# Optimization experiments

Measured on AMD Instinct MI355X. Metric: run time of the kernel, lower is better.

Reference implementation:

```python
import jax, jax.numpy as jnp
import numpy as np
import math

B, L, H, N, OUT, NPRED, NCTRL = 16, 4096, 512, 64, 256, 128, 64


def setup_inputs() -> dict:
    key = jax.random.key(0)
    ks = jax.random.split(key, 12)
    Nh = N // 2
    inp = jax.random.normal(ks[0], (B, L, H), dtype=jnp.float32)
    spec = jax.random.normal(ks[1], (B, L, NCTRL), dtype=jnp.float32)
    # S4DKernel params
    C = jax.random.normal(ks[2], (H, Nh, 2), dtype=jnp.float32)  # view_as_real of cfloat C
    log_dt = (jax.random.uniform(ks[3], (H,), dtype=jnp.float32)
              * (math.log(0.1) - math.log(0.001)) + math.log(0.001))
    log_A_real = jnp.log(0.5 * jnp.ones((H, Nh), dtype=jnp.float32))
    A_imag = math.pi * jnp.broadcast_to(jnp.arange(Nh, dtype=jnp.float32), (H, Nh))
    D = jax.random.normal(ks[4], (H,), dtype=jnp.float32)
    # output_linear: Conv1d(H, 2H, 1) then GLU(dim=-2)
    conv_w = jax.random.normal(ks[5], (2 * H, H), dtype=jnp.float32) / np.sqrt(H)
    conv_b = jax.random.normal(ks[6], (2 * H,), dtype=jnp.float32) * 0.01
    # output: Linear(in_len, out_len) applied on length axis
    out_w = jax.random.normal(ks[7], (OUT, L), dtype=jnp.float32) / np.sqrt(L)
    out_b = jax.random.normal(ks[8], (OUT,), dtype=jnp.float32) * 0.01
    return {"inp": inp, "spec": spec, "C": C, "log_dt": log_dt,
            "log_A_real": log_A_real, "A_imag": A_imag, "D": D,
            "conv_w": conv_w, "conv_b": conv_b, "out_w": out_w, "out_b": out_b}


def s4d_kernel(C, log_dt, log_A_real, A_imag, L):
    # Materialize SSM convolution kernel K: (H, L)
    dt = jnp.exp(log_dt)                                  # (H,)
    Cc = C[..., 0] + 1j * C[..., 1]                       # (H, N/2) complex
    A = -jnp.exp(log_A_real) + 1j * A_imag                # (H, N/2)
    dtA = A * dt[:, None]                                 # (H, N/2)
    # Vandermonde: exp(dtA * l) for l in [0, L)
    V = jnp.exp(dtA[:, :, None] * jnp.arange(L, dtype=jnp.float32))  # (H, N/2, L)
    Cc = Cc * (jnp.exp(dtA) - 1.0) / A                    # (H, N/2)
    K = 2.0 * jnp.einsum('hn,hnl->hl', Cc, V).real        # (H, L)
    return K


def reference(inp, spec, C, log_dt, log_A_real, A_imag, D, conv_w, conv_b, out_w, out_b):
    x = jnp.swapaxes(inp, -1, -2)                         # (B, H, L)
    Lx = x.shape[-1]
    k = s4d_kernel(C, log_dt, log_A_real, A_imag, Lx)     # (H, L)
    # FFT long convolution (linear conv via zero-padding to 2L)
    k_f = jnp.fft.rfft(k, n=2 * Lx)                       # (H, L+1)
    x_f = jnp.fft.rfft(x, n=2 * Lx)                       # (B, H, L+1)
    y = jnp.fft.irfft(x_f * k_f, n=2 * Lx)[..., :Lx]      # (B, H, L)
    y = y + x * D[:, None]                                # skip connection
    y = jax.nn.gelu(y, approximate=False)                 # torch nn.GELU default (erf)
    # Conv1d(k=1) + GLU over channel dim
    z = jnp.einsum('oh,bhl->bol', conv_w, y) + conv_b[:, None]  # (B, 2H, L)
    a, b = z[:, :H, :], z[:, H:, :]
    y = a * jax.nn.sigmoid(b)                             # (B, H, L)
    # Linear over length axis: L -> OUT
    y = jnp.einsum('bhl,ol->bho', y, out_w) + out_b       # (B, H, OUT)
    y = jnp.swapaxes(y, -1, -2)                           # (B, OUT, H)
    return y[:, :OUT, -NPRED:]
```

## Files before the change

### kernel.cpp

```cpp
#include <hip/hip_runtime.h>
#include <hip/hip_bf16.h>
#include <math.h>

#define B_     16
#define L_     4096
#define H_     512
#define NH     32
#define OUT_   256
#define NPRED_ 128
#define CCH    8
#define LCH    512

typedef __attribute__((ext_vector_type(8))) short bf16x8;
typedef __attribute__((ext_vector_type(4))) float f32x4;

__global__ void prep_kernel(const float* __restrict__ conv_w, const float* __restrict__ conv_b,
                            const float* __restrict__ out_w,
                            __hip_bfloat16* __restrict__ Wsel, float* __restrict__ bselp,
                            __hip_bfloat16* __restrict__ outw)
{
    int idx = blockIdx.x * blockDim.x + threadIdx.x;
    if (idx < 256 * 512) {
        int r = idx >> 9, hcol = idx & 511;
        int src = (r < 128) ? (384 + r) : (768 + r);
        Wsel[idx] = __float2bfloat16(conv_w[src * H_ + hcol]);
    } else if (idx < 256 * 512 + 256 * 4096) {
        int i2 = idx - 256 * 512;
        outw[i2] = __float2bfloat16(out_w[i2]);
    } else if (idx < 256 * 512 + 256 * 4096 + 256) {
        int r = idx - 256 * 512 - 256 * 4096;
        int src = (r < 128) ? (384 + r) : (768 + r);
        bselp[r] = conv_b[src];
    }
}

__global__ __launch_bounds__(256)
void scan_pass1(const float* __restrict__ inp, const float* __restrict__ log_dt,
                const float* __restrict__ log_A_real, const float* __restrict__ A_imag,
                float2* __restrict__ M)
{
    const int b = blockIdx.x, hg = blockIdx.y, c = blockIdx.z;
    const int h0 = hg * 32;
    const int tid = threadIdx.x;
    const int q = tid & 7, hl = tid >> 3, h = h0 + hl;

    __shared__ float xs[128][33];

    float wr[4], wi[4], sr[4] = {0,0,0,0}, si[4] = {0,0,0,0};
    const float dt = expf(log_dt[h]);
#pragma unroll
    for (int j = 0; j < 4; ++j) {
        const int n = q * 4 + j;
        const float Ar = -expf(log_A_real[h * NH + n]);
        const float Ai = A_imag[h * NH + n];
        const float er = expf(Ar * dt);
        wr[j] = er * cosf(Ai * dt);
        wi[j] = er * sinf(Ai * dt);
    }

    const size_t base = (size_t)b * L_ * H_ + (size_t)c * LCH * H_ + h0;
    for (int sub = 0; sub < 4; ++sub) {
#pragma unroll
        for (int k = 0; k < 16; ++k) {
            int idx = tid + k * 256;
            int ll = idx >> 5, hh = idx & 31;
            xs[ll][hh] = inp[base + (size_t)(sub * 128 + ll) * H_ + hh];
        }
        __syncthreads();
#pragma unroll 4
        for (int ll = 0; ll < 128; ++ll) {
            const float x = xs[ll][hl];
#pragma unroll
            for (int j = 0; j < 4; ++j) {
                const float nsr = fmaf(wr[j], sr[j], fmaf(-wi[j], si[j], x));
                const float nsi = fmaf(wr[j], si[j], wi[j] * sr[j]);
                sr[j] = nsr; si[j] = nsi;
            }
        }
        __syncthreads();
    }
#pragma unroll
    for (int j = 0; j < 4; ++j)
        M[(((size_t)b * CCH + c) * H_ + h) * NH + q * 4 + j] = make_float2(sr[j], si[j]);
}

__global__ __launch_bounds__(256)
void scan_pass2(const float* __restrict__ log_dt, const float* __restrict__ log_A_real,
                const float* __restrict__ A_imag, const float2* __restrict__ M,
                float2* __restrict__ Sin)
{
    const int idx = blockIdx.x * 256 + threadIdx.x;
    const int n = idx & 31, h = (idx >> 5) & 511, b = idx >> 14;
    const float dt = expf(log_dt[h]);
    const float Ar = -expf(log_A_real[h * NH + n]);
    const float Ai = A_imag[h * NH + n];
    const float er = expf(Ar * dt);
    float wr = er * cosf(Ai * dt), wi = er * sinf(Ai * dt);
#pragma unroll
    for (int s = 0; s < 9; ++s) {
        float nr = wr * wr - wi * wi;
        float ni = 2.0f * wr * wi;
        wr = nr; wi = ni;
    }
    float sre = 0.f, sim = 0.f;
#pragma unroll
    for (int c = 0; c < CCH; ++c) {
        const size_t mi_ = (((size_t)b * CCH + c) * H_ + h) * NH + n;
        float2 m = M[mi_];
        Sin[mi_] = make_float2(sre, sim);
        float nr = fmaf(wr, sre, fmaf(-wi, sim, m.x));
        float ni = fmaf(wr, sim, fmaf(wi, sre, m.y));
        sre = nr; sim = ni;
    }
}

__global__ __launch_bounds__(256)
void scan_pass3(const float* __restrict__ inp, const float* __restrict__ C,
                const float* __restrict__ log_dt, const float* __restrict__ log_A_real,
                const float* __restrict__ A_imag, const float* __restrict__ Dv,
                const float2* __restrict__ Sin, __hip_bfloat16* __restrict__ gT)
{
    const int b = blockIdx.x, hg = blockIdx.y, c = blockIdx.z;
    const int h0 = hg * 32;
    const int tid = threadIdx.x;
    const int q = tid & 7, hl = tid >> 3, h = h0 + hl;

    __shared__ float xs[128][33];
    __shared__ float ys[32][129];
    __shared__ float Ds[32];
    if (tid < 32) Ds[tid] = Dv[h0 + tid];

    const float dt = expf(log_dt[h]);
    float wr[4], wi[4], cr[4], cni[4], sr[4], si[4];
#pragma unroll
    for (int j = 0; j < 4; ++j) {
        const int n = q * 4 + j;
        const float Ar = -expf(log_A_real[h * NH + n]);
        const float Ai = A_imag[h * NH + n];
        const float er = expf(Ar * dt);
        const float wrr = er * cosf(Ai * dt);
        const float wii = er * sinf(Ai * dt);
        const float m2 = Ar * Ar + Ai * Ai;
        const float nr = wrr - 1.0f, nim = wii;
        const float qr = (nr * Ar + nim * Ai) / m2;
        const float qi = (nim * Ar - nr * Ai) / m2;
        const float Cr = C[(h * NH + n) * 2 + 0];
        const float Ci = C[(h * NH + n) * 2 + 1];
        wr[j]  = wrr;  wi[j] = wii;
        cr[j]  =  2.0f * (Cr * qr - Ci * qi);
        cni[j] = -2.0f * (Cr * qi + Ci * qr);
        float2 sv = Sin[(((size_t)b * CCH + c) * H_ + h) * NH + n];
        sr[j] = sv.x; si[j] = sv.y;
    }

    const size_t base = (size_t)b * L_ * H_ + (size_t)c * LCH * H_ + h0;
    __syncthreads();
    for (int sub = 0; sub < 4; ++sub) {
        const int l0 = c * LCH + sub * 128;
#pragma unroll
        for (int k = 0; k < 16; ++k) {
            int idx = tid + k * 256;
            int ll = idx >> 5, hh = idx & 31;
            xs[ll][hh] = inp[base + (size_t)(sub * 128 + ll) * H_ + hh];
        }
        __syncthreads();
#pragma unroll 4
        for (int ll = 0; ll < 128; ++ll) {
            const float x = xs[ll][hl];
            float y = 0.0f;
#pragma unroll
            for (int j = 0; j < 4; ++j) {
                const float nsr = fmaf(wr[j], sr[j], fmaf(-wi[j], si[j], x));
                const float nsi = fmaf(wr[j], si[j], wi[j] * sr[j]);
                sr[j] = nsr; si[j] = nsi;
                y = fmaf(cr[j], nsr, y);
                y = fmaf(cni[j], nsi, y);
            }
            y += __shfl_xor(y, 1);
            y += __shfl_xor(y, 2);
            y += __shfl_xor(y, 4);
            if (q == 0) ys[hl][ll] = y;
        }
        __syncthreads();
#pragma unroll
        for (int k = 0; k < 16; ++k) {
            int idx = tid + k * 256;
            int ll = idx >> 5, hh = idx & 31;
            float v = ys[hh][ll] + Ds[hh] * xs[ll][hh];
            float ge = 0.5f * v * (1.0f + erff(v * 0.70710678f));
            gT[((size_t)b * L_ + l0 + ll) * H_ + h0 + hh] = __float2bfloat16(ge);
        }
        __syncthreads();
    }
}

__device__ __forceinline__ unsigned short bf16bits(float f) {
    __hip_bfloat16 hv = __float2bfloat16(f);
    return *reinterpret_cast<unsigned short*>(&hv);
}

__global__ __launch_bounds__(512)
void gemm1_kernel(const __hip_bfloat16* __restrict__ gT, const __hip_bfloat16* __restrict__ Wsel,
                  const float* __restrict__ bsel, __hip_bfloat16* __restrict__ gated)
{
    const int b  = blockIdx.y;
    const int l0 = blockIdx.x * 128;
    const int tid = threadIdx.x;
    const int wid = tid >> 6, lane = tid & 63;
    const int wrr = wid >> 2;
    const int wcc = wid & 3;
    const int lr  = lane & 15;
    const int lk8 = (lane >> 4) * 8;

    __shared__ short As[128][40];
    __shared__ short Bs[256][40];

    f32x4 acc[4][4];
#pragma unroll
    for (int i = 0; i < 4; ++i)
#pragma unroll
        for (int j = 0; j < 4; ++j) acc[i][j] = (f32x4){0.f, 0.f, 0.f, 0.f};

    const short* gsrc = (const short*)gT + ((size_t)b * L_ + l0) * H_;
    const short* wsrc = (const short*)Wsel;
    const int arow = tid >> 2, aseg = tid & 3;

    for (int ks = 0; ks < 16; ++ks) {
        const int k0 = ks * 32;
        uint4 av  = *(const uint4*)(gsrc + (size_t)arow * H_ + k0 + aseg * 8);
        uint4 bv0 = *(const uint4*)(wsrc + (size_t)arow * 512 + k0 + aseg * 8);
        uint4 bv1 = *(const uint4*)(wsrc + (size_t)(arow + 128) * 512 + k0 + aseg * 8);
        *(uint4*)&As[arow][aseg * 8]       = av;
        *(uint4*)&Bs[arow][aseg * 8]       = bv0;
        *(uint4*)&Bs[arow + 128][aseg * 8] = bv1;
        __syncthreads();

        bf16x8 af[4], bfr[4];
#pragma unroll
        for (int mi = 0; mi < 4; ++mi)
            af[mi] = *(const bf16x8*)&As[wrr * 64 + mi * 16 + lr][lk8];
#pragma unroll
        for (int ni = 0; ni < 4; ++ni) {
            int col = (ni < 2) ? (wcc * 32 + ni * 16) : (128 + wcc * 32 + (ni - 2) * 16);
            bfr[ni] = *(const bf16x8*)&Bs[col + lr][lk8];
        }
#pragma unroll
        for (int mi = 0; mi < 4; ++mi)
#pragma unroll
            for (int ni = 0; ni < 4; ++ni)
                acc[mi][ni] = __builtin_amdgcn_mfma_f32_16x16x32_bf16(af[mi], bfr[ni], acc[mi][ni], 0, 0, 0);
        __syncthreads();
    }

    const int lj4 = (lane >> 4) * 4;
#pragma unroll
    for (int mi = 0; mi < 4; ++mi) {
#pragma unroll
        for (int ni = 0; ni < 2; ++ni) {
            const int oa = wcc * 32 + ni * 16 + lr;
            const float ba  = bsel[oa];
            const float bbv = bsel[oa + 128];
            ushort4 pack;
            unsigned short* pu = (unsigned short*)&pack;
#pragma unroll
            for (int j = 0; j < 4; ++j) {
                float za = acc[mi][ni][j] + ba;
                float zb = acc[mi][ni + 2][j] + bbv;
                float gv = za * (1.0f / (1.0f + expf(-zb)));
                pu[j] = bf16bits(gv);
            }
            const int lrow = l0 + wrr * 64 + mi * 16 + lj4;
            *(ushort4*)((unsigned short*)gated + ((size_t)b * NPRED_ + oa) * L_ + lrow) = pack;
        }
    }
}

__global__ __launch_bounds__(256)
void gemm2_kernel(const __hip_bfloat16* __restrict__ gated, const __hip_bfloat16* __restrict__ outw,
                  const float* __restrict__ outb, float* __restrict__ outp)
{
    const int b  = blockIdx.y;
    const int ot = blockIdx.x & 3, ht = blockIdx.x >> 2;
    const int o0 = ot * 64, hh0 = ht * 64;
    const int tid = threadIdx.x;
    const int wid = tid >> 6, lane = tid & 63;
    const int wrr = wid >> 1;
    const int wcc = wid & 1;
    const int lr  = lane & 15;
    const int lk8 = (lane >> 4) * 8;

    __shared__ short As[64][72];
    __shared__ short Bs[64][72];

    f32x4 acc[2][2];
#pragma unroll
    for (int i = 0; i < 2; ++i)
#pragma unroll
        for (int j = 0; j < 2; ++j) acc[i][j] = (f32x4){0.f, 0.f, 0.f, 0.f};

    const short* asrc = (const short*)gated + ((size_t)b * NPRED_ + hh0) * L_;
    const short* bsrc = (const short*)outw + (size_t)o0 * L_;
    const int row = tid >> 2, seg = tid & 3;

    for (int ks = 0; ks < 64; ++ks) {
        const int k0 = ks * 64;
        uint4 a0 = *(const uint4*)(asrc + (size_t)row * L_ + k0 + seg * 8);
        uint4 a1 = *(const uint4*)(asrc + (size_t)row * L_ + k0 + 32 + seg * 8);
        uint4 b0 = *(const uint4*)(bsrc + (size_t)row * L_ + k0 + seg * 8);
        uint4 b1 = *(const uint4*)(bsrc + (size_t)row * L_ + k0 + 32 + seg * 8);
        __syncthreads();
        *(uint4*)&As[row][seg * 8]      = a0;
        *(uint4*)&As[row][32 + seg * 8] = a1;
        *(uint4*)&Bs[row][seg * 8]      = b0;
        *(uint4*)&Bs[row][32 + seg * 8] = b1;
        __syncthreads();

#pragma unroll
        for (int kk = 0; kk < 2; ++kk) {
            bf16x8 af[2], bfv[2];
#pragma unroll
            for (int mi = 0; mi < 2; ++mi)
                af[mi] = *(const bf16x8*)&As[wrr * 32 + mi * 16 + lr][kk * 32 + lk8];
#pragma unroll
            for (int ni = 0; ni < 2; ++ni)
                bfv[ni] = *(const bf16x8*)&Bs[wcc * 32 + ni * 16 + lr][kk * 32 + lk8];
#pragma unroll
            for (int mi = 0; mi < 2; ++mi)
#pragma unroll
                for (int ni = 0; ni < 2; ++ni)
                    acc[mi][ni] = __builtin_amdgcn_mfma_f32_16x16x32_bf16(af[mi], bfv[ni], acc[mi][ni], 0, 0, 0);
        }
    }

    const int lj4 = (lane >> 4) * 4;
#pragma unroll
    for (int mi = 0; mi < 2; ++mi) {
#pragma unroll
        for (int ni = 0; ni < 2; ++ni) {
            const int og = o0 + wcc * 32 + ni * 16 + lr;
            const float bo = outb[og];
            float4 v;
            v.x = acc[mi][ni][0] + bo;
            v.y = acc[mi][ni][1] + bo;
            v.z = acc[mi][ni][2] + bo;
            v.w = acc[mi][ni][3] + bo;
            const int hh = hh0 + wrr * 32 + mi * 16 + lj4;
            *(float4*)(outp + ((size_t)b * OUT_ + og) * NPRED_ + hh) = v;
        }
    }
}

extern "C" void kernel_launch(void* const* d_in, const int* in_sizes, int n_in,
                              void* d_out, int out_size, void* d_ws, size_t ws_size,
                              hipStream_t stream)
{
    const float* inp        = (const float*)d_in[0];
    const float* C          = (const float*)d_in[2];
    const float* log_dt     = (const float*)d_in[3];
    const float* log_A_real = (const float*)d_in[4];
    const float* A_imag     = (const float*)d_in[5];
    const float* Dv         = (const float*)d_in[6];
    const float* conv_w     = (const float*)d_in[7];
    const float* conv_b     = (const float*)d_in[8];
    const float* out_w      = (const float*)d_in[9];
    const float* out_b      = (const float*)d_in[10];
    float* outp = (float*)d_out;

    const size_t off_Wsel  = 0;
    const size_t off_outw  = 262144;
    const size_t off_bsel  = 2359296;
    const size_t off_gT    = 2360320;
    const size_t off_gated = 69469184;
    const size_t off_M     = off_gT;
    const size_t off_Sin   = off_gated;
    const size_t need      = 86246400;
    if (ws_size < need) return;

    char* ws = (char*)d_ws;
    __hip_bfloat16* Wsel  = (__hip_bfloat16*)(ws + off_Wsel);
    __hip_bfloat16* outw  = (__hip_bfloat16*)(ws + off_outw);
    float*          bselp = (float*)(ws + off_bsel);
    __hip_bfloat16* gT    = (__hip_bfloat16*)(ws + off_gT);
    __hip_bfloat16* gated = (__hip_bfloat16*)(ws + off_gated);
    float2*         M     = (float2*)(ws + off_M);
    float2*         Sin   = (float2*)(ws + off_Sin);

    const int prep_total = 256 * 512 + 256 * 4096 + 256;
    prep_kernel<<<(prep_total + 255) / 256, 256, 0, stream>>>(conv_w, conv_b, out_w, Wsel, bselp, outw);
    scan_pass1<<<dim3(16, 16, CCH), 256, 0, stream>>>(inp, log_dt, log_A_real, A_imag, M);
    scan_pass2<<<1024, 256, 0, stream>>>(log_dt, log_A_real, A_imag, M, Sin);
    scan_pass3<<<dim3(16, 16, CCH), 256, 0, stream>>>(inp, C, log_dt, log_A_real, A_imag, Dv, Sin, gT);
    gemm1_kernel<<<dim3(32, 16), 512, 0, stream>>>(gT, Wsel, bselp, gated);
    gemm2_kernel<<<dim3(8, 16), 256, 0, stream>>>(gated, outw, out_b, outp);
}
```

Before: 612.6 us.

## Remap scan threads to 16 modes per lane and drop shared-memory staging

Reworks the chunked SSM scan kernels so each wavefront owns one length chunk, with each lane holding 16 complex modes for one channel instead of 4. Inputs are read directly from global memory through a small register prefetch queue, which removes the shared-memory tiles and block barriers. In pass 3 the output reduction becomes a single cross-half shuffle, and GELU is written straight to gT per row. Pass 2 now updates M in place, so the separate Sin buffer is gone. The cost is higher register pressure (about 96 live floats per thread), 32-wide strided global loads per row, and fewer blocks in the launch grid.

Result: slower. 808.2 us (+31.9%).

```diff
diff --git a/kernel.cpp b/kernel.cpp
--- a/kernel.cpp
+++ b/kernel.cpp
@@ -39,55 +39,56 @@
                 const float* __restrict__ log_A_real, const float* __restrict__ A_imag,
                 float2* __restrict__ M)
 {
-    const int b = blockIdx.x, hg = blockIdx.y, c = blockIdx.z;
-    const int h0 = hg * 32;
+    const int b = blockIdx.x, hg = blockIdx.y, cq = blockIdx.z;
     const int tid = threadIdx.x;
-    const int q = tid & 7, hl = tid >> 3, h = h0 + hl;
-
-    __shared__ float xs[128][33];
-
-    float wr[4], wi[4], sr[4] = {0,0,0,0}, si[4] = {0,0,0,0};
+    const int wv = tid >> 6, lane = tid & 63;
+    const int c = cq * 4 + wv;
+    const int hl = lane & 31, nh0 = (lane >> 5) * 16;
+    const int h = hg * 32 + hl;
+
+    float wr[16], wi[16], sr[16], si[16];
     const float dt = expf(log_dt[h]);
 #pragma unroll
-    for (int j = 0; j < 4; ++j) {
-        const int n = q * 4 + j;
+    for (int j = 0; j < 16; ++j) {
+        const int n = nh0 + j;
         const float Ar = -expf(log_A_real[h * NH + n]);
         const float Ai = A_imag[h * NH + n];
         const float er = expf(Ar * dt);
         wr[j] = er * cosf(Ai * dt);
         wi[j] = er * sinf(Ai * dt);
-    }
-
-    const size_t base = (size_t)b * L_ * H_ + (size_t)c * LCH * H_ + h0;
-    for (int sub = 0; sub < 4; ++sub) {
-#pragma unroll
-        for (int k = 0; k < 16; ++k) {
-            int idx = tid + k * 256;
-            int ll = idx >> 5, hh = idx & 31;
-            xs[ll][hh] = inp[base + (size_t)(sub * 128 + ll) * H_ + hh];
-        }
-        __syncthreads();
+        sr[j] = 0.f; si[j] = 0.f;
+    }
+
+    const float* xp = inp + ((size_t)b * L_ + (size_t)c * LCH) * H_ + h;
+    float xq0 = xp[0 * (size_t)H_];
+    float xq1 = xp[1 * (size_t)H_];
+    float xq2 = xp[2 * (size_t)H_];
+    float xq3 = xp[3 * (size_t)H_];
 #pragma unroll 4
-        for (int ll = 0; ll < 128; ++ll) {
-            const float x = xs[ll][hl];
-#pragma unroll
-            for (int j = 0; j < 4; ++j) {
-                const float nsr = fmaf(wr[j], sr[j], fmaf(-wi[j], si[j], x));
-                const float nsi = fmaf(wr[j], si[j], wi[j] * sr[j]);
-                sr[j] = nsr; si[j] = nsi;
-            }
-        }
-        __syncthreads();
-    }
-#pragma unroll
-    for (int j = 0; j < 4; ++j)
-        M[(((size_t)b * CCH + c) * H_ + h) * NH + q * 4 + j] = make_float2(sr[j], si[j]);
+    for (int l = 0; l < LCH; ++l) {
+        int lp = l + 4; lp = (lp < LCH) ? lp : (LCH - 1);
+        const float xf = xp[(size_t)lp * H_];
+        const float x = xq0;
+#pragma unroll
+        for (int j = 0; j < 16; ++j) {
+            const float nsr = fmaf(wr[j], sr[j], fmaf(-wi[j], si[j], x));
+            const float nsi = fmaf(wr[j], si[j], wi[j] * sr[j]);
+            sr[j] = nsr; si[j] = nsi;
+        }
+        xq0 = xq1; xq1 = xq2; xq2 = xq3; xq3 = xf;
+    }
+
+    float2* Mp = M + (((size_t)b * CCH + c) * H_ + h) * NH + nh0;
+#pragma unroll
+    for (int j = 0; j < 16; j += 2) {
+        float4 v; v.x = sr[j]; v.y = si[j]; v.z = sr[j + 1]; v.w = si[j + 1];
+        *(float4*)&Mp[j] = v;
+    }
 }
 
 __global__ __launch_bounds__(256)
 void scan_pass2(const float* __restrict__ log_dt, const float* __restrict__ log_A_real,
-                const float* __restrict__ A_imag, const float2* __restrict__ M,
-                float2* __restrict__ Sin)
+                const float* __restrict__ A_imag, float2* __restrict__ M)
 {
     const int idx = blockIdx.x * 256 + threadIdx.x;
     const int n = idx & 31, h = (idx >> 5) & 511, b = idx >> 14;
@@ -107,7 +108,7 @@
     for (int c = 0; c < CCH; ++c) {
         const size_t mi_ = (((size_t)b * CCH + c) * H_ + h) * NH + n;
         float2 m = M[mi_];
-        Sin[mi_] = make_float2(sre, sim);
+        M[mi_] = make_float2(sre, sim);
         float nr = fmaf(wr, sre, fmaf(-wi, sim, m.x));
         float ni = fmaf(wr, sim, fmaf(wi, sre, m.y));
         sre = nr; sim = ni;
@@ -120,21 +121,19 @@
                 const float* __restrict__ A_imag, const float* __restrict__ Dv,
                 const float2* __restrict__ Sin, __hip_bfloat16* __restrict__ gT)
 {
-    const int b = blockIdx.x, hg = blockIdx.y, c = blockIdx.z;
-    const int h0 = hg * 32;
+    const int b = blockIdx.x, hg = blockIdx.y, cq = blockIdx.z;
     const int tid = threadIdx.x;
-    const int q = tid & 7, hl = tid >> 3, h = h0 + hl;
-
-    __shared__ float xs[128][33];
-    __shared__ float ys[32][129];
-    __shared__ float Ds[32];
-    if (tid < 32) Ds[tid] = Dv[h0 + tid];
-
+    const int wv = tid >> 6, lane = tid & 63;
+    const int c = cq * 4 + wv;
+    const int hl = lane & 31, nh0 = (lane >> 5) * 16;
+    const int h = hg * 32 + hl;
+
+    float wr[16], wi[16], cr[16], cni[16], sr[16], si[16];
     const float dt = expf(log_dt[h]);
-    float wr[4], wi[4], cr[4], cni[4], sr[4], si[4];
-#pragma unroll
-    for (int j = 0; j < 4; ++j) {
-        const int n = q * 4 + j;
+    const float2* Sp = Sin + (((size_t)b * CCH + c) * H_ + h) * NH + nh0;
+#pragma unroll
+    for (int j = 0; j < 16; ++j) {
+        const int n = nh0 + j;
         const float Ar = -expf(log_A_real[h * NH + n]);
         const float Ai = A_imag[h * NH + n];
         const float er = expf(Ar * dt);
@@ -149,48 +148,37 @@
         wr[j]  = wrr;  wi[j] = wii;
         cr[j]  =  2.0f * (Cr * qr - Ci * qi);
         cni[j] = -2.0f * (Cr * qi + Ci * qr);
-        float2 sv = Sin[(((size_t)b * CCH + c) * H_ + h) * NH + n];
+        float2 sv = Sp[j];
         sr[j] = sv.x; si[j] = sv.y;
     }
-
-    const size_t base = (size_t)b * L_ * H_ + (size_t)c * LCH * H_ + h0;
-    __syncthreads();
-    for (int sub = 0; sub < 4; ++sub) {
-        const int l0 = c * LCH + sub * 128;
-#pragma unroll
-        for (int k = 0; k < 16; ++k) {
-            int idx = tid + k * 256;
-            int ll = idx >> 5, hh = idx & 31;
-            xs[ll][hh] = inp[base + (size_t)(sub * 128 + ll) * H_ + hh];
-        }
-        __syncthreads();
-#pragma unroll 4
-        for (int ll = 0; ll < 128; ++ll) {
-            const float x = xs[ll][hl];
-            float y = 0.0f;
-#pragma unroll
-            for (int j = 0; j < 4; ++j) {
-                const float nsr = fmaf(wr[j], sr[j], fmaf(-wi[j], si[j], x));
-                const float nsi = fmaf(wr[j], si[j], wi[j] * sr[j]);
-                sr[j] = nsr; si[j] = nsi;
-                y = fmaf(cr[j], nsr, y);
-                y = fmaf(cni[j], nsi, y);
-            }
-            y += __shfl_xor(y, 1);
-            y += __shfl_xor(y, 2);
-            y += __shfl_xor(y, 4);
-            if (q == 0) ys[hl][ll] = y;
-        }
-        __syncthreads();
-#pragma unroll
-        for (int k = 0; k < 16; ++k) {
-            int idx = tid + k * 256;
-            int ll = idx >> 5, hh = idx & 31;
-            float v = ys[hh][ll] + Ds[hh] * xs[ll][hh];
-            float ge = 0.5f * v * (1.0f + erff(v * 0.70710678f));
-            gT[((size_t)b * L_ + l0 + ll) * H_ + h0 + hh] = __float2bfloat16(ge);
-        }
-        __syncthreads();
+    const float Dh = Dv[h];
+
+    const float* xp = inp + ((size_t)b * L_ + (size_t)c * LCH) * H_ + h;
+    __hip_bfloat16* gp = gT + ((size_t)b * L_ + (size_t)c * LCH) * H_ + h;
+
+    float xq0 = xp[0 * (size_t)H_];
+    float xq1 = xp[1 * (size_t)H_];
+    float xq2 = xp[2 * (size_t)H_];
+    float xq3 = xp[3 * (size_t)H_];
+#pragma unroll 2
+    for (int l = 0; l < LCH; ++l) {
+        int lp = l + 4; lp = (lp < LCH) ? lp : (LCH - 1);
+        const float xf = xp[(size_t)lp * H_];
+        const float x = xq0;
+        float y = 0.0f;
+#pragma unroll
+        for (int j = 0; j < 16; ++j) {
+            const float nsr = fmaf(wr[j], sr[j], fmaf(-wi[j], si[j], x));
+            const float nsi = fmaf(wr[j], si[j], wi[j] * sr[j]);
+            sr[j] = nsr; si[j] = nsi;
+            y = fmaf(cr[j], nsr, y);
+            y = fmaf(cni[j], nsi, y);
+        }
+        y += __shfl_xor(y, 32);
+        const float v = fmaf(Dh, x, y);
+        const float ge = 0.5f * v * (1.0f + erff(v * 0.70710678f));
+        if (lane < 32) gp[(size_t)l * H_] = __float2bfloat16(ge);
+        xq0 = xq1; xq1 = xq2; xq2 = xq3; xq3 = xf;
     }
 }
 
@@ -371,8 +359,7 @@
     const size_t off_bsel  = 2359296;
     const size_t off_gT    = 2360320;
     const size_t off_gated = 69469184;
-    const size_t off_M     = off_gT;
-    const size_t off_Sin   = off_gated;
+    const size_t off_M     = off_gated;
     const size_t need      = 86246400;
     if (ws_size < need) return;
 
@@ -383,13 +370,12 @@
     __hip_bfloat16* gT    = (__hip_bfloat16*)(ws + off_gT);
     __hip_bfloat16* gated = (__hip_bfloat16*)(ws + off_gated);
     float2*         M     = (float2*)(ws + off_M);
-    float2*         Sin   = (float2*)(ws + off_Sin);
 
     const int prep_total = 256 * 512 + 256 * 4096 + 256;
     prep_kernel<<<(prep_total + 255) / 256, 256, 0, stream>>>(conv_w, conv_b, out_w, Wsel, bselp, outw);
-    scan_pass1<<<dim3(16, 16, CCH), 256, 0, stream>>>(inp, log_dt, log_A_real, A_imag, M);
-    scan_pass2<<<1024, 256, 0, stream>>>(log_dt, log_A_real, A_imag, M, Sin);
-    scan_pass3<<<dim3(16, 16, CCH), 256, 0, stream>>>(inp, C, log_dt, log_A_real, A_imag, Dv, Sin, gT);
+    scan_pass1<<<dim3(16, 16, 2), 256, 0, stream>>>(inp, log_dt, log_A_real, A_imag, M);
+    scan_pass2<<<1024, 256, 0, stream>>>(log_dt, log_A_real, A_imag, M);
+    scan_pass3<<<dim3(16, 16, 2), 256, 0, stream>>>(inp, C, log_dt, log_A_real, A_imag, Dv, M, gT);
     gemm1_kernel<<<dim3(32, 16), 512, 0, stream>>>(gT, Wsel, bselp, gated);
     gemm2_kernel<<<dim3(8, 16), 256, 0, stream>>>(gated, outw, out_b, outp);
 }
```
